# Kernel optimization log

Measured on AMD Instinct MI355X. Metric: run time of the kernel, lower is better.

Reference implementation:

```python
import jax, jax.numpy as jnp
import numpy as np

B, D, F, M = 4096, 768, 16384, 256

def setup_inputs() -> dict:
    key = jax.random.key(0)
    ks = jax.random.split(key, 5)
    return {
        "x": jax.random.normal(ks[0], (B, D), dtype=jnp.float32),
        "memory_bank": jax.random.normal(ks[1], (F, D), dtype=jnp.float32),
        "W_q": jax.random.normal(ks[2], (M, D), dtype=jnp.float32) / np.sqrt(D),
        "b_q": jnp.zeros((M,), dtype=jnp.float32),
        "W_k": jax.random.normal(ks[3], (M, D), dtype=jnp.float32) / np.sqrt(D),
        "b_k": jnp.zeros((M,), dtype=jnp.float32),
        "W_v": jax.random.normal(ks[4], (D, D), dtype=jnp.float32) / np.sqrt(D),
        "b_v": jnp.zeros((D,), dtype=jnp.float32),
        "temperature": jnp.full((1,), np.sqrt(M / 4.0), dtype=jnp.float32),
    }

def reference(x, memory_bank, W_q, b_q, W_k, b_k, W_v, b_v, temperature):
    # Q from x, K/V from fixed memory bank (torch Linear: y = x @ W.T + b)
    Q = x @ W_q.T + b_q                     # [B, M]
    K = memory_bank @ W_k.T + b_k           # [F, M]
    V = memory_bank @ W_v.T + b_v           # [F, D]
    scores = (Q @ K.T) / temperature        # [B, F]
    f = jax.nn.softmax(scores, axis=1)      # max-subtraction folded into stable softmax
    x_hat = f @ V                           # [B, D]
    return (x, x_hat, f, V)
```

## Files before the change

### kernel.cpp

```cpp
#include <hip/hip_runtime.h>
#include <stdint.h>

#define B_ 4096
#define D_ 768
#define F_ 16384
#define M_ 256

typedef short bf16x8 __attribute__((ext_vector_type(8)));
typedef float f32x4 __attribute__((ext_vector_type(4)));
typedef unsigned short ushort8 __attribute__((ext_vector_type(8)));

__device__ __forceinline__ unsigned short f2bf(float f) {
  union { float f; uint32_t u; } c; c.f = f;
  uint32_t u = c.u;
  uint32_t r = (u + 0x7FFFu + ((u >> 16) & 1u)) >> 16;
  return (unsigned short)r;
}

__device__ __forceinline__ float bf2f(unsigned short s) {
  union { uint32_t u; float f; } c; c.u = ((uint32_t)s) << 16;
  return c.f;
}

__device__ __forceinline__ void gl_lds16(const void* g, void* l) {
  __builtin_amdgcn_global_load_lds(
      (const __attribute__((address_space(1))) unsigned int*)g,
      (__attribute__((address_space(3))) unsigned int*)l, 16, 0, 0);
}

__global__ void cast_kernel(const float* __restrict__ in, unsigned short* __restrict__ out,
                            float* __restrict__ cpy, int n4) {
  int i = blockIdx.x * blockDim.x + threadIdx.x;
  if (i >= n4) return;
  float4 v = reinterpret_cast<const float4*>(in)[i];
  ushort4 u;
  u.x = f2bf(v.x); u.y = f2bf(v.y); u.z = f2bf(v.z); u.w = f2bf(v.w);
  reinterpret_cast<ushort4*>(out)[i] = u;
  if (cpy) reinterpret_cast<float4*>(cpy)[i] = v;
}

template <int EPI>
__global__ __launch_bounds__(256, 2) void gemm_bt(
    const unsigned short* __restrict__ A, const unsigned short* __restrict__ Bm,
    const float* __restrict__ bias, float* __restrict__ Cf,
    unsigned short* __restrict__ Cb, int M, int N, int K,
    float* __restrict__ rowsum, const float* __restrict__ tptr) {
  __shared__ unsigned short As[128 * 32];
  __shared__ unsigned short Bs[128 * 32];
  const int tid = threadIdx.x, lane = tid & 63, wave = tid >> 6;
  const int m0 = blockIdx.y * 128, n0 = blockIdx.x * 128;
  const int wr = wave >> 1, wc = wave & 1;
  const int q = lane >> 4;
  f32x4 acc[4][4] = {};

  for (int k0 = 0; k0 < K; k0 += 32) {
#pragma unroll
    for (int i = 0; i < 2; ++i) {
      int cb = (i * 4 + wave) * 64;
      int ch = cb + lane;
      int row = ch >> 2, ko = (ch & 3) * 8;
      gl_lds16(A + (size_t)(m0 + row) * K + k0 + ko, (char*)As + (size_t)cb * 16);
      gl_lds16(Bm + (size_t)(n0 + row) * K + k0 + ko, (char*)Bs + (size_t)cb * 16);
    }
    __syncthreads();
    bf16x8 a[4];
#pragma unroll
    for (int m = 0; m < 4; ++m)
      a[m] = *reinterpret_cast<const bf16x8*>(
          &As[(wr * 64 + m * 16 + (lane & 15)) * 32 + q * 8]);
#pragma unroll
    for (int n = 0; n < 4; ++n) {
      bf16x8 b = *reinterpret_cast<const bf16x8*>(
          &Bs[(wc * 64 + n * 16 + (lane & 15)) * 32 + q * 8]);
#pragma unroll
      for (int m = 0; m < 4; ++m)
        acc[m][n] = __builtin_amdgcn_mfma_f32_16x16x32_bf16(a[m], b, acc[m][n], 0, 0, 0);
    }
    __syncthreads();
  }

  const int rbase = m0 + wr * 64 + q * 4;
  const int cbase = n0 + wc * 64 + (lane & 15);
  if constexpr (EPI == 3) {
    __shared__ unsigned short Cs[128 * 128];
    const float invt = 1.0f / tptr[0];
    const int rl0 = wr * 64 + q * 4, cl0 = wc * 64 + (lane & 15);
#pragma unroll
    for (int m = 0; m < 4; ++m) {
      float rs[4] = {0.f, 0.f, 0.f, 0.f};
#pragma unroll
      for (int n = 0; n < 4; ++n) {
#pragma unroll
        for (int r = 0; r < 4; ++r) {
          float e = __expf(acc[m][n][r] * invt);
          rs[r] += e;
          Cs[(rl0 + m * 16 + r) * 128 + cl0 + n * 16] = f2bf(e);
        }
      }
#pragma unroll
      for (int r = 0; r < 4; ++r) {
        float s = rs[r];
        s += __shfl_xor(s, 1);
        s += __shfl_xor(s, 2);
        s += __shfl_xor(s, 4);
        s += __shfl_xor(s, 8);
        if ((lane & 15) == 0) atomicAdd(&rowsum[rbase + m * 16 + r], s);
      }
    }
    __syncthreads();
    const size_t ebase = ((size_t)(m0 >> 7) * 512 + (n0 >> 5)) * 4096;
#pragma unroll
    for (int j = 0; j < 8; ++j) {
      int u = j * 256 + tid;
      int tl = u >> 9, r = (u >> 2) & 127, p = u & 3;
      ushort8 v = *reinterpret_cast<const ushort8*>(
          &Cs[r * 128 + tl * 32 + ((p ^ ((r >> 1) & 3)) * 8)]);
      *reinterpret_cast<ushort8*>(&Cb[ebase + (size_t)tl * 4096 + r * 32 + p * 8]) = v;
    }
  } else if constexpr (EPI == 2) {
    const float invt = 1.0f / tptr[0];
#pragma unroll
    for (int m = 0; m < 4; ++m) {
      float rs[4] = {0.f, 0.f, 0.f, 0.f};
#pragma unroll
      for (int n = 0; n < 4; ++n) {
        int col = cbase + n * 16;
#pragma unroll
        for (int r = 0; r < 4; ++r) {
          float e = __expf(acc[m][n][r] * invt);
          Cf[(size_t)(rbase + m * 16 + r) * N + col] = e;
          rs[r] += e;
        }
      }
#pragma unroll
      for (int r = 0; r < 4; ++r) {
        float s = rs[r];
        s += __shfl_xor(s, 1);
        s += __shfl_xor(s, 2);
        s += __shfl_xor(s, 4);
        s += __shfl_xor(s, 8);
        if ((lane & 15) == 0) atomicAdd(&rowsum[rbase + m * 16 + r], s);
      }
    }
  } else {
#pragma unroll
    for (int m = 0; m < 4; ++m) {
#pragma unroll
      for (int n = 0; n < 4; ++n) {
        int col = cbase + n * 16;
        float bv = bias[col];
#pragma unroll
        for (int r = 0; r < 4; ++r) {
          float v = acc[m][n][r] + bv;
          size_t idx = (size_t)(rbase + m * 16 + r) * N + col;
          if (EPI == 0) Cb[idx] = f2bf(v);
          else Cf[idx] = v;
        }
      }
    }
  }
}

__global__ __launch_bounds__(256) void vt_tiler(const float* __restrict__ V,
                                                unsigned short* __restrict__ Vt_tiled) {
  __shared__ unsigned short T[768][36];
  const int t = blockIdx.x, k0 = t * 32, tid = threadIdx.x;
  const int kl = tid >> 3, c0 = (tid & 7) * 4;
  for (int cb = 0; cb < 768; cb += 32) {
    float4 v = *reinterpret_cast<const float4*>(&V[(size_t)(k0 + kl) * D_ + cb + c0]);
    T[cb + c0 + 0][kl] = f2bf(v.x);
    T[cb + c0 + 1][kl] = f2bf(v.y);
    T[cb + c0 + 2][kl] = f2bf(v.z);
    T[cb + c0 + 3][kl] = f2bf(v.w);
  }
  __syncthreads();
  for (int d = tid; d < 768; d += 256) {
    const int x = (d >> 1) & 3;
    unsigned short* o = Vt_tiled + (size_t)t * 24576 + d * 32;
#pragma unroll
    for (int s = 0; s < 4; ++s) {
      ushort4 lo = *reinterpret_cast<const ushort4*>(&T[d][(s ^ x) * 8]);
      ushort4 hi = *reinterpret_cast<const ushort4*>(&T[d][(s ^ x) * 8 + 4]);
      *reinterpret_cast<ushort4*>(o + s * 8) = lo;
      *reinterpret_cast<ushort4*>(o + s * 8 + 4) = hi;
    }
  }
}

__global__ __launch_bounds__(512, 4) void xhat_clean(
    const unsigned short* __restrict__ Et, const unsigned short* __restrict__ Vtt,
    const float* __restrict__ rowsum, unsigned short* __restrict__ partial) {
  __shared__ unsigned short As[2][128 * 32];
  __shared__ unsigned short Bs[2][192 * 32];
  const int tid = threadIdx.x, lane = tid & 63, wave = tid >> 6;
  const int combo = blockIdx.x & 15, mb = blockIdx.x >> 4;
  const int ks = combo >> 2, nb = combo & 3;
  const int q = lane >> 4;
  const int wr = wave >> 2, wc = wave & 3;
  const int t0 = ks * 128;
  f32x4 acc[4][3] = {};

  const unsigned short* abase =
      Et + ((size_t)mb * 512 + t0) * 4096 + lane * 8;
  const unsigned short* bbase =
      Vtt + (size_t)t0 * 24576 + nb * 6144 + lane * 8;

  for (int si = 0; si < 64; ++si) {
    const size_t tA = (size_t)(2 * si) * 4096;
    const size_t tB = (size_t)(2 * si) * 24576;
    if (wave < 4) {
#pragma unroll
      for (int j = 0; j < 4; ++j) {
        int c = wave * 4 + j;
        int h = c >> 3, cw = c & 7;
        gl_lds16(abase + tA + (size_t)h * 4096 + cw * 512,
                 (char*)As + h * 8192 + cw * 1024);
      }
    } else {
#pragma unroll
      for (int j = 0; j < 6; ++j) {
        int c = (wave - 4) * 6 + j;
        int h = c / 12, cc = c % 12;
        gl_lds16(bbase + tB + (size_t)h * 24576 + cc * 512,
                 (char*)Bs + h * 12288 + cc * 1024);
      }
    }
    __syncthreads();
#pragma unroll
    for (int h = 0; h < 2; ++h) {
      bf16x8 a[4], b[3];
#pragma unroll
      for (int m = 0; m < 4; ++m) {
        int R = wr * 64 + m * 16 + (lane & 15);
        a[m] = *reinterpret_cast<const bf16x8*>(
            &As[h][R * 32 + ((q ^ ((R >> 1) & 3)) * 8)]);
      }
#pragma unroll
      for (int n = 0; n < 3; ++n) {
        int C = wc * 48 + n * 16 + (lane & 15);
        b[n] = *reinterpret_cast<const bf16x8*>(
            &Bs[h][C * 32 + ((q ^ ((C >> 1) & 3)) * 8)]);
      }
#pragma unroll
      for (int n = 0; n < 3; ++n)
#pragma unroll
        for (int m = 0; m < 4; ++m)
          acc[m][n] = __builtin_amdgcn_mfma_f32_16x16x32_bf16(a[m], b[n], acc[m][n], 0, 0, 0);
    }
    __syncthreads();
  }

  unsigned short* P = partial + (size_t)ks * B_ * D_;
#pragma unroll
  for (int m = 0; m < 4; ++m) {
    int rowb = mb * 128 + wr * 64 + m * 16 + q * 4;
#pragma unroll
    for (int r = 0; r < 4; ++r) {
      float inv = 1.0f / rowsum[rowb + r];
      size_t ro = (size_t)(rowb + r) * D_;
#pragma unroll
      for (int n = 0; n < 3; ++n) {
        int col = nb * 192 + wc * 48 + n * 16 + (lane & 15);
        P[ro + col] = f2bf(acc[m][n][r] * inv);
      }
    }
  }
}

__global__ __launch_bounds__(256) void normalize_f(
    const unsigned short* __restrict__ Et, const float* __restrict__ rowsum,
    float* __restrict__ f) {
  int u = blockIdx.x * blockDim.x + threadIdx.x;
  int g = u >> 9, w = u & 511;
  int r = w >> 2, p = w & 3;
  int rb = g >> 9, t = g & 511;
  int row = rb * 128 + r;
  int col = t * 32 + (p ^ ((r >> 1) & 3)) * 8;
  float inv = 1.0f / rowsum[row];
  ushort8 e = *reinterpret_cast<const ushort8*>(&Et[(size_t)g * 4096 + w * 8]);
  float4 o0, o1;
  o0.x = bf2f(e[0]) * inv; o0.y = bf2f(e[1]) * inv;
  o0.z = bf2f(e[2]) * inv; o0.w = bf2f(e[3]) * inv;
  o1.x = bf2f(e[4]) * inv; o1.y = bf2f(e[5]) * inv;
  o1.z = bf2f(e[6]) * inv; o1.w = bf2f(e[7]) * inv;
  float* fp = &f[(size_t)row * F_ + col];
  *reinterpret_cast<float4*>(fp) = o0;
  *reinterpret_cast<float4*>(fp + 4) = o1;
}

__global__ __launch_bounds__(512, 4) void xhat_v4(
    float* __restrict__ Ef, const unsigned short* __restrict__ Vt_tiled,
    const float* __restrict__ rowsum, unsigned short* __restrict__ partial) {
  __shared__ unsigned short As2[64 * 32];
  __shared__ unsigned short Vs[768 * 32];
  const int tid = threadIdx.x, lane = tid & 63, wave = tid >> 6;
  const int ks = blockIdx.x & 7, rb = blockIdx.x >> 3;
  const int r0 = rb * 64;
  const int kbeg = ks * (F_ / 8);
  const int wr = wave >> 2, wc = wave & 3;
  const int erow = tid >> 3, ec = (tid & 7) * 4;
  const float inv_f = 1.0f / rowsum[r0 + erow];
  const int q = lane >> 4;
  f32x4 acc[2][12] = {};

  float* ep = Ef + (size_t)(r0 + erow) * F_ + kbeg + ec;
  float4 e = *reinterpret_cast<const float4*>(ep);
  const int NSTEP = (F_ / 8) / 32;
  const unsigned short* vt_base =
      Vt_tiled + (size_t)(kbeg >> 5) * 24576 + wave * 512 + lane * 8;

  for (int si = 0; si < NSTEP; ++si) {
    float4 f4 = make_float4(e.x * inv_f, e.y * inv_f, e.z * inv_f, e.w * inv_f);
    *reinterpret_cast<float4*>(ep) = f4;
    ushort4 u;
    u.x = f2bf(e.x); u.y = f2bf(e.y); u.z = f2bf(e.z); u.w = f2bf(e.w);
    {
      int slot = ec >> 3, off = ec & 7;
      *reinterpret_cast<ushort4*>(
          &As2[erow * 32 + ((slot ^ ((erow >> 1) & 3)) * 8) + off]) = u;
    }
    const unsigned short* vs_src = vt_base + (size_t)si * 24576;
#pragma unroll
    for (int j = 0; j < 6; ++j)
      gl_lds16(vs_src + j * 4096, (char*)Vs + (size_t)(j * 512 + wave * 64) * 16);
    __syncthreads();
    if (si + 1 < NSTEP) e = *reinterpret_cast<const float4*>(ep + 32);
    ep += 32;
    bf16x8 a[2];
#pragma unroll
    for (int m = 0; m < 2; ++m) {
      int R = wr * 32 + m * 16 + (lane & 15);
      a[m] = *reinterpret_cast<const bf16x8*>(&As2[R * 32 + ((q ^ ((R >> 1) & 3)) * 8)]);
    }
#pragma unroll
    for (int n = 0; n < 12; ++n) {
      int C = wc * 192 + n * 16 + (lane & 15);
      bf16x8 b = *reinterpret_cast<const bf16x8*>(&Vs[C * 32 + ((q ^ ((C >> 1) & 3)) * 8)]);
      acc[0][n] = __builtin_amdgcn_mfma_f32_16x16x32_bf16(a[0], b, acc[0][n], 0, 0, 0);
      acc[1][n] = __builtin_amdgcn_mfma_f32_16x16x32_bf16(a[1], b, acc[1][n], 0, 0, 0);
    }
    __syncthreads();
  }

  unsigned short* P = partial + (size_t)ks * B_ * D_;
#pragma unroll
  for (int m = 0; m < 2; ++m) {
    int rowb = r0 + wr * 32 + m * 16 + q * 4;
#pragma unroll
    for (int r = 0; r < 4; ++r) {
      float inv = 1.0f / rowsum[rowb + r];
      size_t row_off = (size_t)(rowb + r) * D_;
#pragma unroll
      for (int n = 0; n < 12; ++n) {
        int col = wc * 192 + n * 16 + (lane & 15);
        P[row_off + col] = f2bf(acc[m][n][r] * inv);
      }
    }
  }
}

__global__ void reduce_kernel(const unsigned short* __restrict__ partial,
                              float* __restrict__ out, int n8, int nks) {
  int i = blockIdx.x * blockDim.x + threadIdx.x;
  if (i >= n8) return;
  size_t base = (size_t)i * 8;
  float s[8] = {0.f, 0.f, 0.f, 0.f, 0.f, 0.f, 0.f, 0.f};
  for (int ks = 0; ks < nks; ++ks) {
    ushort8 v = *reinterpret_cast<const ushort8*>(&partial[(size_t)ks * B_ * D_ + base]);
#pragma unroll
    for (int j = 0; j < 8; ++j) s[j] += bf2f(v[j]);
  }
  float4 o0 = make_float4(s[0], s[1], s[2], s[3]);
  float4 o1 = make_float4(s[4], s[5], s[6], s[7]);
  *reinterpret_cast<float4*>(&out[base]) = o0;
  *reinterpret_cast<float4*>(&out[base + 4]) = o1;
}

extern "C" void kernel_launch(void* const* d_in, const int* in_sizes, int n_in,
                              void* d_out, int out_size, void* d_ws, size_t ws_size,
                              hipStream_t stream) {
  const float* x = (const float*)d_in[0];
  const float* mb = (const float*)d_in[1];
  const float* Wq = (const float*)d_in[2];
  const float* bq = (const float*)d_in[3];
  const float* Wk = (const float*)d_in[4];
  const float* bk = (const float*)d_in[5];
  const float* Wv = (const float*)d_in[6];
  const float* bv = (const float*)d_in[7];
  const float* temp = (const float*)d_in[8];

  float* out_x = (float*)d_out;
  float* out_xhat = out_x + (size_t)B_ * D_;
  float* out_f = out_xhat + (size_t)B_ * D_;
  float* out_V = out_f + (size_t)B_ * F_;

  char* ws = (char*)d_ws;
  const size_t WS_NEED_NEW = 195051520;

  if (ws_size >= WS_NEED_NEW) {
    unsigned short* Qb  = (unsigned short*)(ws + 0);
    unsigned short* Kb  = (unsigned short*)(ws + 2097152);
    unsigned short* Vtt = (unsigned short*)(ws + 10485760);
    float* rowsum       = (float*)(ws + 35651584);
    char* A0 = ws + 35667968;
    unsigned short* xb  = (unsigned short*)(A0 + 0);
    unsigned short* mbb = (unsigned short*)(A0 + 6291456);
    unsigned short* Wqb = (unsigned short*)(A0 + 31457280);
    unsigned short* Wkb = (unsigned short*)(A0 + 31850496);
    unsigned short* Wvb = (unsigned short*)(A0 + 32243712);
    unsigned short* Et  = (unsigned short*)A0;
    unsigned short* partial = (unsigned short*)(ws + 169885696);

    hipMemsetAsync(rowsum, 0, B_ * sizeof(float), stream);

    cast_kernel<<<(B_ * D_ / 4 + 255) / 256, 256, 0, stream>>>(x, xb, out_x, B_ * D_ / 4);
    cast_kernel<<<(F_ * D_ / 4 + 255) / 256, 256, 0, stream>>>(mb, mbb, nullptr, F_ * D_ / 4);
    cast_kernel<<<(M_ * D_ / 4 + 255) / 256, 256, 0, stream>>>(Wq, Wqb, nullptr, M_ * D_ / 4);
    cast_kernel<<<(M_ * D_ / 4 + 255) / 256, 256, 0, stream>>>(Wk, Wkb, nullptr, M_ * D_ / 4);
    cast_kernel<<<(D_ * D_ / 4 + 255) / 256, 256, 0, stream>>>(Wv, Wvb, nullptr, D_ * D_ / 4);

    dim3 blk(256);
    gemm_bt<0><<<dim3(M_ / 128, B_ / 128), blk, 0, stream>>>(xb, Wqb, bq, nullptr, Qb,
                                                             B_, M_, D_, nullptr, nullptr);
    gemm_bt<0><<<dim3(M_ / 128, F_ / 128), blk, 0, stream>>>(mbb, Wkb, bk, nullptr, Kb,
                                                             F_, M_, D_, nullptr, nullptr);
    gemm_bt<1><<<dim3(D_ / 128, F_ / 128), blk, 0, stream>>>(mbb, Wvb, bv, out_V, nullptr,
                                                             F_, D_, D_, nullptr, nullptr);
    vt_tiler<<<dim3(F_ / 32), 256, 0, stream>>>(out_V, Vtt);
    gemm_bt<3><<<dim3(F_ / 128, B_ / 128), blk, 0, stream>>>(Qb, Kb, nullptr, nullptr, Et,
                                                             B_, F_, M_, rowsum, temp);
    normalize_f<<<dim3(B_ * F_ / 8 / 256), 256, 0, stream>>>(Et, rowsum, out_f);
    xhat_clean<<<dim3(512), dim3(512), 0, stream>>>(Et, Vtt, rowsum, partial);
    reduce_kernel<<<(B_ * D_ / 8 + 255) / 256, 256, 0, stream>>>(partial, out_xhat,
                                                                 B_ * D_ / 8, 4);
  } else {
    unsigned short* xb  = (unsigned short*)(ws + 0);
    unsigned short* mbb = (unsigned short*)(ws + 6291456);
    unsigned short* Wqb = (unsigned short*)(ws + 31457280);
    unsigned short* Wkb = (unsigned short*)(ws + 31850496);
    unsigned short* Wvb = (unsigned short*)(ws + 32243712);
    unsigned short* Qb  = (unsigned short*)(ws + 33423360);
    unsigned short* Kb  = (unsigned short*)(ws + 35520512);
    unsigned short* Vtt = (unsigned short*)(ws + 43909120);
    float* rowsum       = (float*)(ws + 69074944);
    unsigned short* partial = (unsigned short*)(ws + 69091328);

    hipMemsetAsync(rowsum, 0, B_ * sizeof(float), stream);

    cast_kernel<<<(B_ * D_ / 4 + 255) / 256, 256, 0, stream>>>(x, xb, out_x, B_ * D_ / 4);
    cast_kernel<<<(F_ * D_ / 4 + 255) / 256, 256, 0, stream>>>(mb, mbb, nullptr, F_ * D_ / 4);
    cast_kernel<<<(M_ * D_ / 4 + 255) / 256, 256, 0, stream>>>(Wq, Wqb, nullptr, M_ * D_ / 4);
    cast_kernel<<<(M_ * D_ / 4 + 255) / 256, 256, 0, stream>>>(Wk, Wkb, nullptr, M_ * D_ / 4);
    cast_kernel<<<(D_ * D_ / 4 + 255) / 256, 256, 0, stream>>>(Wv, Wvb, nullptr, D_ * D_ / 4);

    dim3 blk(256);
    gemm_bt<0><<<dim3(M_ / 128, B_ / 128), blk, 0, stream>>>(xb, Wqb, bq, nullptr, Qb,
                                                             B_, M_, D_, nullptr, nullptr);
    gemm_bt<0><<<dim3(M_ / 128, F_ / 128), blk, 0, stream>>>(mbb, Wkb, bk, nullptr, Kb,
                                                             F_, M_, D_, nullptr, nullptr);
    gemm_bt<1><<<dim3(D_ / 128, F_ / 128), blk, 0, stream>>>(mbb, Wvb, bv, out_V, nullptr,
                                                             F_, D_, D_, nullptr, nullptr);
    vt_tiler<<<dim3(F_ / 32), 256, 0, stream>>>(out_V, Vtt);
    gemm_bt<2><<<dim3(F_ / 128, B_ / 128), blk, 0, stream>>>(Qb, Kb, nullptr, out_f, nullptr,
                                                             B_, F_, M_, rowsum, temp);
    xhat_v4<<<dim3(512), dim3(512), 0, stream>>>(out_f, Vtt, rowsum, partial);
    reduce_kernel<<<(B_ * D_ / 8 + 255) / 256, 256, 0, stream>>>(partial, out_xhat,
                                                                 B_ * D_ / 8, 8);
  }
}
```

Measured before the change: 464.0 us.

## Widen x_hat GEMM tile to full D with 8-way split-K and double buffering

The f@V kernel now has each block compute all 768 output columns for 128 rows, using an 8-way split over F instead of a 4x4 split over K and N. This removes the repeated reads of the E tiles across column blocks. The main loop becomes a single-barrier double-buffered pipeline that prefetches the next stage while computing the current one. In exchange, LDS use and the accumulator register count (48 f32x4 per thread) grow a lot, only 256 blocks launch, and the partial buffer and reduction double to 8 slices.

```diff
diff --git a/kernel.cpp b/kernel.cpp
--- a/kernel.cpp
+++ b/kernel.cpp
@@ -187,68 +187,61 @@
   }
 }
 
-__global__ __launch_bounds__(512, 4) void xhat_clean(
+__global__ __launch_bounds__(512, 2) void xhat_v8(
     const unsigned short* __restrict__ Et, const unsigned short* __restrict__ Vtt,
     const float* __restrict__ rowsum, unsigned short* __restrict__ partial) {
   __shared__ unsigned short As[2][128 * 32];
-  __shared__ unsigned short Bs[2][192 * 32];
+  __shared__ unsigned short Bs[2][768 * 32];
   const int tid = threadIdx.x, lane = tid & 63, wave = tid >> 6;
-  const int combo = blockIdx.x & 15, mb = blockIdx.x >> 4;
-  const int ks = combo >> 2, nb = combo & 3;
+  const int ks = blockIdx.x & 7, mb = blockIdx.x >> 3;
   const int q = lane >> 4;
   const int wr = wave >> 2, wc = wave & 3;
-  const int t0 = ks * 128;
-  f32x4 acc[4][3] = {};
-
-  const unsigned short* abase =
-      Et + ((size_t)mb * 512 + t0) * 4096 + lane * 8;
-  const unsigned short* bbase =
-      Vtt + (size_t)t0 * 24576 + nb * 6144 + lane * 8;
-
+  const int t0 = ks * 64;
+  f32x4 acc[4][12] = {};
+
+  const unsigned short* abase = Et + ((size_t)mb * 512 + t0) * 4096 + lane * 8;
+  const unsigned short* bbase = Vtt + (size_t)t0 * 24576 + lane * 8;
+
+#define XH_STAGE(si, buf)                                                     \
+  {                                                                           \
+    _Pragma("unroll")                                                         \
+    for (int j = 0; j < 7; ++j) {                                             \
+      int c = wave * 7 + j;                                                   \
+      if (c < 8)                                                              \
+        gl_lds16(abase + (size_t)(si) * 4096 + c * 512,                       \
+                 (char*)&As[buf][0] + c * 1024);                              \
+      else                                                                    \
+        gl_lds16(bbase + (size_t)(si) * 24576 + (c - 8) * 512,                \
+                 (char*)&Bs[buf][0] + (c - 8) * 1024);                        \
+    }                                                                         \
+  }
+
+  XH_STAGE(0, 0);
+  __syncthreads();
+  int cur = 0;
   for (int si = 0; si < 64; ++si) {
-    const size_t tA = (size_t)(2 * si) * 4096;
-    const size_t tB = (size_t)(2 * si) * 24576;
-    if (wave < 4) {
-#pragma unroll
-      for (int j = 0; j < 4; ++j) {
-        int c = wave * 4 + j;
-        int h = c >> 3, cw = c & 7;
-        gl_lds16(abase + tA + (size_t)h * 4096 + cw * 512,
-                 (char*)As + h * 8192 + cw * 1024);
-      }
-    } else {
-#pragma unroll
-      for (int j = 0; j < 6; ++j) {
-        int c = (wave - 4) * 6 + j;
-        int h = c / 12, cc = c % 12;
-        gl_lds16(bbase + tB + (size_t)h * 24576 + cc * 512,
-                 (char*)Bs + h * 12288 + cc * 1024);
-      }
-    }
-    __syncthreads();
-#pragma unroll
-    for (int h = 0; h < 2; ++h) {
-      bf16x8 a[4], b[3];
-#pragma unroll
-      for (int m = 0; m < 4; ++m) {
-        int R = wr * 64 + m * 16 + (lane & 15);
-        a[m] = *reinterpret_cast<const bf16x8*>(
-            &As[h][R * 32 + ((q ^ ((R >> 1) & 3)) * 8)]);
-      }
-#pragma unroll
-      for (int n = 0; n < 3; ++n) {
-        int C = wc * 48 + n * 16 + (lane & 15);
-        b[n] = *reinterpret_cast<const bf16x8*>(
-            &Bs[h][C * 32 + ((q ^ ((C >> 1) & 3)) * 8)]);
-      }
-#pragma unroll
-      for (int n = 0; n < 3; ++n)
-#pragma unroll
-        for (int m = 0; m < 4; ++m)
-          acc[m][n] = __builtin_amdgcn_mfma_f32_16x16x32_bf16(a[m], b[n], acc[m][n], 0, 0, 0);
-    }
-    __syncthreads();
-  }
+    const int nxt = cur ^ 1;
+    if (si + 1 < 64) XH_STAGE(si + 1, nxt);
+    bf16x8 a[4];
+#pragma unroll
+    for (int m = 0; m < 4; ++m) {
+      int R = wr * 64 + m * 16 + (lane & 15);
+      a[m] = *reinterpret_cast<const bf16x8*>(
+          &As[cur][R * 32 + ((q ^ ((R >> 1) & 3)) * 8)]);
+    }
+#pragma unroll
+    for (int n = 0; n < 12; ++n) {
+      int C = wc * 192 + n * 16 + (lane & 15);
+      bf16x8 b = *reinterpret_cast<const bf16x8*>(
+          &Bs[cur][C * 32 + ((q ^ ((C >> 1) & 3)) * 8)]);
+#pragma unroll
+      for (int m = 0; m < 4; ++m)
+        acc[m][n] = __builtin_amdgcn_mfma_f32_16x16x32_bf16(a[m], b, acc[m][n], 0, 0, 0);
+    }
+    __syncthreads();
+    cur = nxt;
+  }
+#undef XH_STAGE
 
   unsigned short* P = partial + (size_t)ks * B_ * D_;
 #pragma unroll
@@ -259,8 +252,8 @@
       float inv = 1.0f / rowsum[rowb + r];
       size_t ro = (size_t)(rowb + r) * D_;
 #pragma unroll
-      for (int n = 0; n < 3; ++n) {
-        int col = nb * 192 + wc * 48 + n * 16 + (lane & 15);
+      for (int n = 0; n < 12; ++n) {
+        int col = wc * 192 + n * 16 + (lane & 15);
         P[ro + col] = f2bf(acc[m][n][r] * inv);
       }
     }
@@ -395,7 +388,7 @@
   float* out_V = out_f + (size_t)B_ * F_;
 
   char* ws = (char*)d_ws;
-  const size_t WS_NEED_NEW = 195051520;
+  const size_t WS_NEED_NEW = 220217344;
 
   if (ws_size >= WS_NEED_NEW) {
     unsigned short* Qb  = (unsigned short*)(ws + 0);
@@ -430,9 +423,9 @@
     gemm_bt<3><<<dim3(F_ / 128, B_ / 128), blk, 0, stream>>>(Qb, Kb, nullptr, nullptr, Et,
                                                              B_, F_, M_, rowsum, temp);
     normalize_f<<<dim3(B_ * F_ / 8 / 256), 256, 0, stream>>>(Et, rowsum, out_f);
-    xhat_clean<<<dim3(512), dim3(512), 0, stream>>>(Et, Vtt, rowsum, partial);
+    xhat_v8<<<dim3(256), dim3(512), 0, stream>>>(Et, Vtt, rowsum, partial);
     reduce_kernel<<<(B_ * D_ / 8 + 255) / 256, 256, 0, stream>>>(partial, out_xhat,
-                                                                 B_ * D_ / 8, 4);
+                                                                 B_ * D_ / 8, 8);
   } else {
     unsigned short* xb  = (unsigned short*)(ws + 0);
     unsigned short* mbb = (unsigned short*)(ws + 6291456);
```

Measured after the change: 492.7 us. 1.06x slower.
